# Kernel tuning notes

Measured on AMD Instinct MI355X. Metric: run time of the kernel, lower is better.

Reference implementation:

```python
import jax, jax.numpy as jnp
import numpy as np


def _retain(o1, others, W, bias):
    # o1: (b, s, h); others: (b, 4, s, h); W: (h, h); bias: (1,)
    q = o1 @ W                                        # (b, s, h)
    scores = jnp.einsum('bih,bkjh->bijk', q, others) + bias[0]  # (b, s1, s2, 4)
    w = jax.nn.softmax(scores, axis=-1)               # softmax over the 4 options
    # weight[:, :, :, k] @ option_k summed over k
    return jnp.einsum('bijk,bkjh->bih', w, others)


def setup_inputs() -> dict:
    key = jax.random.key(0)
    ks = jax.random.split(key, 7)
    b, s, h = 32, 256, 1024
    opts = {f'option{i+1}': jax.random.normal(ks[i], (b, s, h), dtype=jnp.float32)
            for i in range(5)}
    W = 0.02 * jax.random.normal(ks[5], (h, h), dtype=jnp.float32)
    bias = 0.02 * jax.random.normal(ks[6], (1,), dtype=jnp.float32)
    return {**opts, 'W': W, 'bias': bias}


def reference(option1, option2, option3, option4, option5, W, bias):
    opts = [option1, option2, option3, option4, option5]
    total = None
    for i in range(5):
        others = jnp.stack([opts[j] for j in range(5) if j != i], axis=1)  # (b,4,s,h)
        r = _retain(opts[i], others, W, bias)
        total = r if total is None else total + r
    return total / 2.0
```

## Files before the change

kernel.cpp:

```cpp
#include <hip/hip_runtime.h>
#include <hip/hip_bf16.h>
#include <stdint.h>


#define BB 32
#define SS 256
#define HH 1024

typedef __attribute__((ext_vector_type(4))) float f32x4;
typedef __attribute__((ext_vector_type(8))) __bf16 bf16x8;
typedef __attribute__((ext_vector_type(4))) __bf16 bf16x4;

__device__ constexpr int PAIR(int i, int n) { return i * 4 + (n > i ? n - 1 : n); }

__device__ __forceinline__ void gload_lds16(const void* g, void* l) {
  __builtin_amdgcn_global_load_lds((const __attribute__((address_space(1))) void*)g,
                                   (__attribute__((address_space(3))) void*)l, 16, 0, 0);
}

__global__ void canary(float* out, float v) { out[0] = v; }

__global__ __launch_bounds__(256) void cast_all(
    const float* p0, const float* p1, const float* p2, const float* p3, const float* p4,
    __bf16* __restrict__ dst)
{
  int m = blockIdx.x >> 12;
  long off = ((long)(blockIdx.x & 4095) * 256 + threadIdx.x) * 8;
  const float* src = m == 0 ? p0 : m == 1 ? p1 : m == 2 ? p2 : m == 3 ? p3 : p4;
  float4 v0 = *(const float4*)(src + off);
  float4 v1 = *(const float4*)(src + off + 4);
  bf16x8 h;
  h[0] = (__bf16)v0.x; h[1] = (__bf16)v0.y; h[2] = (__bf16)v0.z; h[3] = (__bf16)v0.w;
  h[4] = (__bf16)v1.x; h[5] = (__bf16)v1.y; h[6] = (__bf16)v1.z; h[7] = (__bf16)v1.w;
  *(bf16x8*)(dst + (long)m * BB * SS * HH + off) = h;
}

__global__ __launch_bounds__(256) void cast_trW(const float* __restrict__ src,
                                                __bf16* __restrict__ dstT)
{
  __shared__ __bf16 tile[64][72];
  int ct = blockIdx.x & 15, rt = blockIdx.x >> 4;
  const float* s = src + (long)(rt * 64) * 1024 + ct * 64;
  int t = threadIdx.x;
#pragma unroll
  for (int p = 0; p < 4; p++) {
    int c = t + p * 256;
    int row = c >> 4, c4 = c & 15;
    float4 v = *(const float4*)(s + (long)row * 1024 + c4 * 4);
    bf16x4 h;
    h[0] = (__bf16)v.x; h[1] = (__bf16)v.y; h[2] = (__bf16)v.z; h[3] = (__bf16)v.w;
    *(bf16x4*)&tile[row][c4 * 4] = h;
  }
  __syncthreads();
#pragma unroll
  for (int p = 0; p < 4; p++) {
    int c = t + p * 256;
    int hr = c >> 4, s4 = c & 15;
    bf16x4 h;
    h[0] = tile[s4 * 4 + 0][hr];
    h[1] = tile[s4 * 4 + 1][hr];
    h[2] = tile[s4 * 4 + 2][hr];
    h[3] = tile[s4 * 4 + 3][hr];
    *(bf16x4*)(dstT + (long)(ct * 64 + hr) * 1024 + rt * 64 + s4 * 4) = h;
  }
}

__global__ __launch_bounds__(512, 2) void qgemm256(
    const __bf16* __restrict__ A, const __bf16* __restrict__ Bt, __bf16* __restrict__ C)
{
  __shared__ __align__(16) char ldsb[2 * 65536];
  int lin = blockIdx.x;
  int xcd = lin & 7, idx = lin >> 3;
  int rt = xcd * 20 + (idx >> 2), ct = idx & 3;
  int t = threadIdx.x, l = t & 63, w = t >> 6;
  int wr = w >> 2, wc = w & 3;
  f32x4 acc[8][4] = {};

  const char* gp[8];
  int dstp[8];
#pragma unroll
  for (int p = 0; p < 8; p++) {
    int c = t + 512 * (p & 3);
    int row = c >> 3;
    int sg = (c & 7) ^ (row & 7);
    if (p < 4) {
      gp[p] = (const char*)(A + (long)(rt * 256 + row) * 1024 + sg * 8);
      dstp[p] = w * 1024 + (p & 3) * 8192;
    } else {
      gp[p] = (const char*)(Bt + (long)(ct * 256 + row) * 1024 + sg * 8);
      dstp[p] = 32768 + w * 1024 + (p & 3) * 8192;
    }
  }

  int lr = l & 15, sl = l >> 4;
  int sx0 = (sl ^ (lr & 7)) * 16;
  int sx1 = ((4 | sl) ^ (lr & 7)) * 16;
  int arow = (wr * 128 + lr) * 128;
  int brow = 32768 + (wc * 64 + lr) * 128;

#define TILE(CUR, DOSTAGE)                                                             \
  {                                                                                    \
    const char* base = ldsb + (CUR) * 65536;                                           \
    char* sbase = ldsb + ((CUR) ^ 1) * 65536;                                          \
    bf16x8 bfr[4][2], af[2][2];                                                        \
    _Pragma("unroll") for (int j = 0; j < 4; j++) {                                    \
      bfr[j][0] = *(const bf16x8*)(base + brow + j * 2048 + sx0);                      \
      bfr[j][1] = *(const bf16x8*)(base + brow + j * 2048 + sx1);                      \
    }                                                                                  \
    _Pragma("unroll") for (int ph = 0; ph < 4; ph++) {                                 \
      if (DOSTAGE) {                                                                   \
        gload_lds16(gp[ph], sbase + dstp[ph]);                                         \
        gload_lds16(gp[ph + 4], sbase + dstp[ph + 4]);                                 \
      }                                                                                \
      _Pragma("unroll") for (int ii = 0; ii < 2; ii++) {                               \
        int i = ph * 2 + ii;                                                           \
        af[ii][0] = *(const bf16x8*)(base + arow + i * 2048 + sx0);                    \
        af[ii][1] = *(const bf16x8*)(base + arow + i * 2048 + sx1);                    \
      }                                                                                \
      __builtin_amdgcn_s_setprio(1);                                                   \
      _Pragma("unroll") for (int ii = 0; ii < 2; ii++)                                 \
        _Pragma("unroll") for (int j = 0; j < 4; j++) {                                \
          acc[ph * 2 + ii][j] = __builtin_amdgcn_mfma_f32_16x16x32_bf16(               \
              af[ii][0], bfr[j][0], acc[ph * 2 + ii][j], 0, 0, 0);                     \
          acc[ph * 2 + ii][j] = __builtin_amdgcn_mfma_f32_16x16x32_bf16(               \
              af[ii][1], bfr[j][1], acc[ph * 2 + ii][j], 0, 0, 0);                     \
        }                                                                              \
      __builtin_amdgcn_s_setprio(0);                                                   \
    }                                                                                  \
    if (DOSTAGE) {                                                                     \
      _Pragma("unroll") for (int p = 0; p < 8; p++) gp[p] += 128;                      \
    }                                                                                  \
  }

  {
#pragma unroll
    for (int p = 0; p < 8; p++) {
      gload_lds16(gp[p], ldsb + dstp[p]);
      gp[p] += 128;
    }
  }
  asm volatile("s_waitcnt vmcnt(0)" ::: "memory");
  __builtin_amdgcn_s_barrier();
  for (int tt = 0; tt < 15; tt++) {
    TILE(tt & 1, 1)
    asm volatile("s_waitcnt vmcnt(0)" ::: "memory");
    __builtin_amdgcn_s_barrier();
  }
  TILE(1, 0)
#undef TILE

#pragma unroll
  for (int i = 0; i < 8; i++) {
    long mrow = (long)rt * 256 + wr * 128 + i * 16 + (sl << 2);
#pragma unroll
    for (int j = 0; j < 4; j++) {
      int n = ct * 256 + wc * 64 + j * 16 + lr;
#pragma unroll
      for (int r = 0; r < 4; r++)
        C[(mrow + r) * 1024 + n] = (__bf16)acc[i][j][r];
    }
  }
}

__global__ __launch_bounds__(512, 2) void gram64(
    const __bf16* __restrict__ Q, const __bf16* __restrict__ O, __bf16* __restrict__ V)
{
  __shared__ __align__(16) char ldsb[3 * 40960];
  int bid = blockIdx.x;
  int xcd = bid & 7, idx = bid >> 3;
  int b = xcd * 4 + (idx >> 4);
  int rem = idx & 15;
  int s1t = rem >> 2, s2t = rem & 3;
  int t = threadIdx.x, l = t & 63, w = t >> 6;
  int wr = w >> 1, wc = w & 1;
  f32x4 acc[20][2] = {};

  const char* gp[5];
#pragma unroll
  for (int p = 0; p < 5; p++) {
    int c = t + 512 * p;
    int isQ = c < 1280;
    int cc = isQ ? c : c - 1280;
    int m = cc >> 8, rr = (cc >> 2) & 63;
    int sg = (cc & 3) ^ ((cc >> 3) & 3);
    long row = (long)m * (BB * SS) + (long)b * SS + (isQ ? s1t : s2t) * 64 + rr;
    gp[p] = (const char*)((isQ ? Q : O) + row * HH + sg * 8);
  }
  int dstb = (t & ~63) << 4;

#define STAGE(BUF)                                                      \
  {                                                                     \
    char* base = ldsb + (BUF) * 40960 + dstb;                           \
    _Pragma("unroll") for (int p = 0; p < 5; p++) {                     \
      gload_lds16(gp[p], base + p * 8192);                              \
      gp[p] += 64;                                                      \
    }                                                                   \
  }

  int lr = l & 15, sl = l >> 4;
  int swz = (sl ^ ((lr >> 1) & 3)) * 16;
  int qoff = (wr * 16 + lr) * 64 + swz;
  int ooff0 = 20480 + (wc * 32 + lr) * 64 + swz;
  int ooff1 = ooff0 + 1024;

#define COMPUTE(BUF)                                                                   \
  {                                                                                    \
    const char* base = ldsb + (BUF) * 40960;                                           \
    bf16x8 qf[5], of[5];                                                               \
    _Pragma("unroll") for (int m = 0; m < 5; m++)                                      \
      qf[m] = *(const bf16x8*)(base + m * 4096 + qoff);                                \
    _Pragma("unroll") for (int m = 0; m < 5; m++)                                      \
      of[m] = *(const bf16x8*)(base + m * 4096 + ooff0);                               \
    __builtin_amdgcn_s_setprio(1);                                                     \
    _Pragma("unroll") for (int i = 0; i < 5; i++) {                                    \
      _Pragma("unroll") for (int n = 0; n < 5; n++) {                                  \
        if (n != i)                                                                    \
          acc[PAIR(i, n)][0] = __builtin_amdgcn_mfma_f32_16x16x32_bf16(                \
              qf[i], of[n], acc[PAIR(i, n)][0], 0, 0, 0);                              \
      }                                                                                \
    }                                                                                  \
    __builtin_amdgcn_s_setprio(0);                                                     \
    _Pragma("unroll") for (int m = 0; m < 5; m++)                                      \
      of[m] = *(const bf16x8*)(base + m * 4096 + ooff1);                               \
    __builtin_amdgcn_s_setprio(1);                                                     \
    _Pragma("unroll") for (int i = 0; i < 5; i++) {                                    \
      _Pragma("unroll") for (int n = 0; n < 5; n++) {                                  \
        if (n != i)                                                                    \
          acc[PAIR(i, n)][1] = __builtin_amdgcn_mfma_f32_16x16x32_bf16(                \
              qf[i], of[n], acc[PAIR(i, n)][1], 0, 0, 0);                              \
      }                                                                                \
    }                                                                                  \
    __builtin_amdgcn_s_setprio(0);                                                     \
  }

#define STEP(CUR, STG)                                          \
  asm volatile("s_waitcnt vmcnt(5)" ::: "memory");              \
  __builtin_amdgcn_s_barrier();                                 \
  STAGE(STG);                                                   \
  COMPUTE(CUR);

  STAGE(0)
  STAGE(1)
  for (int it = 0; it < 10; it++) {
    STEP(0, 2)
    STEP(1, 0)
    STEP(2, 1)
  }
  asm volatile("s_waitcnt vmcnt(5)" ::: "memory");
  __builtin_amdgcn_s_barrier();
  COMPUTE(0)
  asm volatile("s_waitcnt vmcnt(0)" ::: "memory");
  __builtin_amdgcn_s_barrier();
  COMPUTE(1)
#undef STEP
#undef COMPUTE
#undef STAGE

  int s1b = s1t * 64 + wr * 16 + sl * 4;
  int s2b = s2t * 64 + wc * 32 + lr;
#pragma unroll
  for (int h = 0; h < 2; h++) {
#pragma unroll
    for (int r = 0; r < 4; r++) {
      float vacc[5] = {0.f, 0.f, 0.f, 0.f, 0.f};
#pragma unroll
      for (int i = 0; i < 5; i++) {
        float gg[5];
        float mx = -3.0e38f;
#pragma unroll
        for (int n = 0; n < 5; n++)
          if (n != i) { gg[n] = acc[PAIR(i, n)][h][r]; mx = fmaxf(mx, gg[n]); }
        float ee[5], ssum = 0.f;
#pragma unroll
        for (int n = 0; n < 5; n++)
          if (n != i) { ee[n] = __expf(gg[n] - mx); ssum += ee[n]; }
        float inv = 1.0f / ssum;
#pragma unroll
        for (int n = 0; n < 5; n++)
          if (n != i) vacc[n] += ee[n] * inv;
      }
      int s1 = s1b + r, s2 = s2b + h * 16;
#pragma unroll
      for (int n = 0; n < 5; n++)
        V[((long)(n * BB + b) * SS + s1) * SS + s2] = (__bf16)vacc[n];
    }
  }
}

__global__ __launch_bounds__(256) void pvgemm(
    const __bf16* __restrict__ Vb, const __bf16* __restrict__ Obf, float* __restrict__ out)
{
  __shared__ __bf16 smA[128][40];
  __shared__ __bf16 smB[128][40];
  int bid = blockIdx.x;
  int b = bid >> 4, s1t = (bid >> 3) & 1, ht = bid & 7;
  int t = threadIdx.x, l = t & 63, w = t >> 6;
  int wm = w >> 1, wn = w & 1;
  f32x4 acc[4][4] = {};
#pragma unroll
  for (int n = 0; n < 5; n++) {
    const __bf16* On = Obf + (long)n * BB * SS * HH;
    for (int st2 = 0; st2 < 8; st2++) {
      int s20 = st2 * 32;
#pragma unroll
      for (int p = 0; p < 2; p++) {
        int c = t + p * 256;
        int row = c >> 2, sl = c & 3;
        *(bf16x8*)&smA[row][sl * 8] =
            *(const bf16x8*)(Vb + (long)(n * BB + b) * SS * SS + (long)(s1t * 128 + row) * SS +
                             s20 + sl * 8);
      }
      {
        int h4 = (t & 31) * 4, s2q = (t >> 5) * 4;
        const __bf16* src = On + ((long)b * 256 + s20 + s2q) * 1024 + ht * 128 + h4;
        bf16x4 v0 = *(const bf16x4*)(src);
        bf16x4 v1 = *(const bf16x4*)(src + 1024);
        bf16x4 v2 = *(const bf16x4*)(src + 2048);
        bf16x4 v3 = *(const bf16x4*)(src + 3072);
        bf16x4 c0, c1, c2, c3;
        c0[0] = v0[0]; c0[1] = v1[0]; c0[2] = v2[0]; c0[3] = v3[0];
        c1[0] = v0[1]; c1[1] = v1[1]; c1[2] = v2[1]; c1[3] = v3[1];
        c2[0] = v0[2]; c2[1] = v1[2]; c2[2] = v2[2]; c2[3] = v3[2];
        c3[0] = v0[3]; c3[1] = v1[3]; c3[2] = v2[3]; c3[3] = v3[3];
        *(bf16x4*)&smB[h4 + 0][s2q] = c0;
        *(bf16x4*)&smB[h4 + 1][s2q] = c1;
        *(bf16x4*)&smB[h4 + 2][s2q] = c2;
        *(bf16x4*)&smB[h4 + 3][s2q] = c3;
      }
      __syncthreads();
      bf16x8 af[4], bfr[4];
      int sl = l >> 4, lr = l & 15;
#pragma unroll
      for (int i = 0; i < 4; i++) {
        af[i]  = *(const bf16x8*)&smA[wm * 64 + i * 16 + lr][sl * 8];
        bfr[i] = *(const bf16x8*)&smB[wn * 64 + i * 16 + lr][sl * 8];
      }
#pragma unroll
      for (int i = 0; i < 4; i++)
#pragma unroll
        for (int j = 0; j < 4; j++)
          acc[i][j] = __builtin_amdgcn_mfma_f32_16x16x32_bf16(af[i], bfr[j], acc[i][j], 0, 0, 0);
      __syncthreads();
    }
  }
#pragma unroll
  for (int i = 0; i < 4; i++) {
    int m = s1t * 128 + wm * 64 + i * 16 + ((l >> 4) << 2);
#pragma unroll
    for (int j = 0; j < 4; j++) {
      int n = ht * 128 + wn * 64 + j * 16 + (l & 15);
#pragma unroll
      for (int r = 0; r < 4; r++)
        out[(long)(b * SS + m + r) * HH + n] = 0.5f * acc[i][j][r];
    }
  }
}

extern "C" void kernel_launch(void* const* d_in, const int* in_sizes, int n_in,
                              void* d_out, int out_size, void* d_ws, size_t ws_size,
                              hipStream_t stream)
{
  const size_t SZ_W = (size_t)HH * HH * 2;
  const size_t SZ_Q = (size_t)5 * BB * SS * HH * 2;
  const size_t SZ_V = (size_t)5 * BB * SS * SS * 2;
  const size_t SZ_O = (size_t)5 * BB * SS * HH * 2;
  const size_t NEED = SZ_W + SZ_Q + SZ_V + SZ_O;
  if (ws_size < NEED) {
    canary<<<1, 1, 0, stream>>>((float*)d_out, (float)(ws_size >> 20));
    return;
  }
  char* ws = (char*)d_ws;
  __bf16* Wt  = (__bf16*)ws;
  __bf16* Qb  = (__bf16*)(ws + SZ_W);
  __bf16* Vb  = (__bf16*)(ws + SZ_W + SZ_Q);
  __bf16* Obf = (__bf16*)(ws + SZ_W + SZ_Q + SZ_V);
  const float* o0 = (const float*)d_in[0];
  const float* o1 = (const float*)d_in[1];
  const float* o2 = (const float*)d_in[2];
  const float* o3 = (const float*)d_in[3];
  const float* o4 = (const float*)d_in[4];

  cast_trW<<<256, 256, 0, stream>>>((const float*)d_in[5], Wt);
  cast_all<<<5 * 4096, 256, 0, stream>>>(o0, o1, o2, o3, o4, Obf);
  qgemm256<<<640, 512, 0, stream>>>(Obf, Wt, Qb);
  gram64<<<512, 512, 0, stream>>>(Qb, Obf, Vb);
  pvgemm<<<512, 256, 0, stream>>>(Vb, Obf, (float*)d_out);
}
```

Measured before the change: 262.6 us.

## Replace direct global-to-LDS loads with register-staged double buffering in GEMM kernels

Both the projection GEMM and the Gram kernel stop using global_load_lds DMA and instead load tiles into registers, then write them into swizzled LDS after the compute of the current buffer. The Gram kernel drops from triple to double buffering, which frees LDS. The goal is tighter control of the load/compute overlap and lower LDS footprint. In exchange it adds register pressure (extra bf16x8 staging registers) and an explicit vmcnt(0) wait each iteration that may expose global latency.

```diff
diff --git a/kernel.cpp b/kernel.cpp
--- a/kernel.cpp
+++ b/kernel.cpp
@@ -12,11 +12,6 @@
 typedef __attribute__((ext_vector_type(4))) __bf16 bf16x4;
 
 __device__ constexpr int PAIR(int i, int n) { return i * 4 + (n > i ? n - 1 : n); }
-
-__device__ __forceinline__ void gload_lds16(const void* g, void* l) {
-  __builtin_amdgcn_global_load_lds((const __attribute__((address_space(1))) void*)g,
-                                   (__attribute__((address_space(3))) void*)l, 16, 0, 0);
-}
 
 __global__ void canary(float* out, float v) { out[0] = v; }
 
@@ -77,19 +72,34 @@
   f32x4 acc[8][4] = {};
 
   const char* gp[8];
-  int dstp[8];
+  int wdst[8];
 #pragma unroll
   for (int p = 0; p < 8; p++) {
     int c = t + 512 * (p & 3);
-    int row = c >> 3;
-    int sg = (c & 7) ^ (row & 7);
+    int row = c >> 3, slot = c & 7;
+    int wb = row * 128 + ((slot ^ (row & 7)) << 4);
     if (p < 4) {
-      gp[p] = (const char*)(A + (long)(rt * 256 + row) * 1024 + sg * 8);
-      dstp[p] = w * 1024 + (p & 3) * 8192;
+      gp[p] = (const char*)(A + (long)(rt * 256 + row) * 1024 + slot * 8);
+      wdst[p] = wb;
     } else {
-      gp[p] = (const char*)(Bt + (long)(ct * 256 + row) * 1024 + sg * 8);
-      dstp[p] = 32768 + w * 1024 + (p & 3) * 8192;
+      gp[p] = (const char*)(Bt + (long)(ct * 256 + row) * 1024 + slot * 8);
+      wdst[p] = 32768 + wb;
     }
+  }
+  bf16x8 sreg[8];
+
+#define LOADS                                                     \
+  {                                                               \
+    _Pragma("unroll") for (int p = 0; p < 8; p++) {               \
+      sreg[p] = *(const bf16x8*)gp[p];                            \
+      gp[p] += 128;                                               \
+    }                                                             \
+  }
+#define WRITES(BUF)                                               \
+  {                                                               \
+    char* base = ldsb + (BUF) * 65536;                            \
+    _Pragma("unroll") for (int p = 0; p < 8; p++)                 \
+      *(bf16x8*)(base + wdst[p]) = sreg[p];                       \
   }
 
   int lr = l & 15, sl = l >> 4;
@@ -98,20 +108,15 @@
   int arow = (wr * 128 + lr) * 128;
   int brow = 32768 + (wc * 64 + lr) * 128;
 
-#define TILE(CUR, DOSTAGE)                                                             \
+#define TILE(CUR)                                                                      \
   {                                                                                    \
     const char* base = ldsb + (CUR) * 65536;                                           \
-    char* sbase = ldsb + ((CUR) ^ 1) * 65536;                                          \
     bf16x8 bfr[4][2], af[2][2];                                                        \
     _Pragma("unroll") for (int j = 0; j < 4; j++) {                                    \
       bfr[j][0] = *(const bf16x8*)(base + brow + j * 2048 + sx0);                      \
       bfr[j][1] = *(const bf16x8*)(base + brow + j * 2048 + sx1);                      \
     }                                                                                  \
     _Pragma("unroll") for (int ph = 0; ph < 4; ph++) {                                 \
-      if (DOSTAGE) {                                                                   \
-        gload_lds16(gp[ph], sbase + dstp[ph]);                                         \
-        gload_lds16(gp[ph + 4], sbase + dstp[ph + 4]);                                 \
-      }                                                                                \
       _Pragma("unroll") for (int ii = 0; ii < 2; ii++) {                               \
         int i = ph * 2 + ii;                                                           \
         af[ii][0] = *(const bf16x8*)(base + arow + i * 2048 + sx0);                    \
@@ -127,27 +132,35 @@
         }                                                                              \
       __builtin_amdgcn_s_setprio(0);                                                   \
     }                                                                                  \
-    if (DOSTAGE) {                                                                     \
-      _Pragma("unroll") for (int p = 0; p < 8; p++) gp[p] += 128;                      \
-    }                                                                                  \
-  }
-
-  {
-#pragma unroll
-    for (int p = 0; p < 8; p++) {
-      gload_lds16(gp[p], ldsb + dstp[p]);
-      gp[p] += 128;
-    }
-  }
+  }
+
+#define BODY(CUR, T)                                              \
+  {                                                               \
+    TILE(CUR)                                                     \
+    if ((T) < 15) {                                               \
+      asm volatile("s_waitcnt vmcnt(0)" ::: "memory");            \
+      WRITES((CUR) ^ 1)                                           \
+      if ((T) < 14) { LOADS }                                     \
+    }                                                             \
+    asm volatile("s_waitcnt lgkmcnt(0)" ::: "memory");            \
+    __builtin_amdgcn_s_barrier();                                 \
+  }
+
+  LOADS
   asm volatile("s_waitcnt vmcnt(0)" ::: "memory");
+  WRITES(0)
+  LOADS
+  asm volatile("s_waitcnt lgkmcnt(0)" ::: "memory");
   __builtin_amdgcn_s_barrier();
-  for (int tt = 0; tt < 15; tt++) {
-    TILE(tt & 1, 1)
-    asm volatile("s_waitcnt vmcnt(0)" ::: "memory");
-    __builtin_amdgcn_s_barrier();
-  }
-  TILE(1, 0)
+
+  for (int it = 0; it < 8; it++) {
+    BODY(0, 2 * it)
+    BODY(1, 2 * it + 1)
+  }
+#undef BODY
 #undef TILE
+#undef WRITES
+#undef LOADS
 
 #pragma unroll
   for (int i = 0; i < 8; i++) {
@@ -165,7 +178,7 @@
 __global__ __launch_bounds__(512, 2) void gram64(
     const __bf16* __restrict__ Q, const __bf16* __restrict__ O, __bf16* __restrict__ V)
 {
-  __shared__ __align__(16) char ldsb[3 * 40960];
+  __shared__ __align__(16) char ldsb[2 * 40960];
   int bid = blockIdx.x;
   int xcd = bid & 7, idx = bid >> 3;
   int b = xcd * 4 + (idx >> 4);
@@ -176,25 +189,31 @@
   f32x4 acc[20][2] = {};
 
   const char* gp[5];
+  int wdst[5];
 #pragma unroll
   for (int p = 0; p < 5; p++) {
     int c = t + 512 * p;
     int isQ = c < 1280;
     int cc = isQ ? c : c - 1280;
-    int m = cc >> 8, rr = (cc >> 2) & 63;
-    int sg = (cc & 3) ^ ((cc >> 3) & 3);
+    int m = cc >> 8, rr = (cc >> 2) & 63, slot = cc & 3;
     long row = (long)m * (BB * SS) + (long)b * SS + (isQ ? s1t : s2t) * 64 + rr;
-    gp[p] = (const char*)((isQ ? Q : O) + row * HH + sg * 8);
-  }
-  int dstb = (t & ~63) << 4;
-
-#define STAGE(BUF)                                                      \
-  {                                                                     \
-    char* base = ldsb + (BUF) * 40960 + dstb;                           \
-    _Pragma("unroll") for (int p = 0; p < 5; p++) {                     \
-      gload_lds16(gp[p], base + p * 8192);                              \
-      gp[p] += 64;                                                      \
-    }                                                                   \
+    gp[p] = (const char*)((isQ ? Q : O) + row * HH + slot * 8);
+    wdst[p] = (isQ ? 0 : 20480) + m * 4096 + rr * 64 + ((slot ^ ((rr >> 1) & 3)) << 4);
+  }
+  bf16x8 sreg[5];
+
+#define LOADS                                                     \
+  {                                                               \
+    _Pragma("unroll") for (int p = 0; p < 5; p++) {               \
+      sreg[p] = *(const bf16x8*)gp[p];                            \
+      gp[p] += 64;                                                \
+    }                                                             \
+  }
+#define WRITES(BUF)                                               \
+  {                                                               \
+    char* base = ldsb + (BUF) * 40960;                            \
+    _Pragma("unroll") for (int p = 0; p < 5; p++)                 \
+      *(bf16x8*)(base + wdst[p]) = sreg[p];                       \
   }
 
   int lr = l & 15, sl = l >> 4;
@@ -233,28 +252,33 @@
     __builtin_amdgcn_s_setprio(0);                                                     \
   }
 
-#define STEP(CUR, STG)                                          \
-  asm volatile("s_waitcnt vmcnt(5)" ::: "memory");              \
-  __builtin_amdgcn_s_barrier();                                 \
-  STAGE(STG);                                                   \
-  COMPUTE(CUR);
-
-  STAGE(0)
-  STAGE(1)
-  for (int it = 0; it < 10; it++) {
-    STEP(0, 2)
-    STEP(1, 0)
-    STEP(2, 1)
-  }
-  asm volatile("s_waitcnt vmcnt(5)" ::: "memory");
+#define BODY(CUR, T)                                              \
+  {                                                               \
+    COMPUTE(CUR)                                                  \
+    if ((T) < 31) {                                               \
+      asm volatile("s_waitcnt vmcnt(0)" ::: "memory");            \
+      WRITES((CUR) ^ 1)                                           \
+      if ((T) < 30) { LOADS }                                     \
+    }                                                             \
+    asm volatile("s_waitcnt lgkmcnt(0)" ::: "memory");            \
+    __builtin_amdgcn_s_barrier();                                 \
+  }
+
+  LOADS
+  asm volatile("s_waitcnt vmcnt(0)" ::: "memory");
+  WRITES(0)
+  LOADS
+  asm volatile("s_waitcnt lgkmcnt(0)" ::: "memory");
   __builtin_amdgcn_s_barrier();
-  COMPUTE(0)
-  asm volatile("s_waitcnt vmcnt(0)" ::: "memory");
-  __builtin_amdgcn_s_barrier();
-  COMPUTE(1)
-#undef STEP
+
+  for (int it = 0; it < 16; it++) {
+    BODY(0, 2 * it)
+    BODY(1, 2 * it + 1)
+  }
+#undef BODY
 #undef COMPUTE
-#undef STAGE
+#undef WRITES
+#undef LOADS
 
   int s1b = s1t * 64 + wr * 16 + sl * 4;
   int s2b = s2t * 64 + wc * 32 + lr;
```

Result: slower. 274.4 us (+4.5%).
